# Performance work log

Measured on AMD Instinct MI355X. Metric: run time of the kernel, lower is better.

## Reference

```python
import jax, jax.numpy as jnp
import numpy as np

MAX_S, MIN_S, MAX_R = 3.0, 0.5, 3.0
A = (MAX_S - MIN_S) / 2.0   # 1.25
B = (MAX_S + MIN_S) / 2.0   # 1.75
C = (MAX_R - 1.0) / 2.0     # 1.0
D = (MAX_R + 1.0) / 2.0     # 2.0

# 3x3 kernel base points, row-major: dim0 = dy, dim1 = dx, shape [2, 9]
BASE = jnp.array([[-1, -1], [-1, 0], [-1, 1], [0, -1], [0, 0], [0, 1],
                  [1, -1], [1, 0], [1, 1]], dtype=jnp.float32).T


def conv2d(x, w, b=None):
    y = jax.lax.conv_general_dilated(x, w, window_strides=(1, 1),
                                     padding=((1, 1), (1, 1)),
                                     dimension_numbers=('NCHW', 'OIHW', 'NCHW'))
    if b is not None:
        y = y + b[None, :, None, None]
    return y


def setup_inputs() -> dict:
    key = jax.random.key(0)
    ks = jax.random.split(key, 8)
    return {
        'x': jax.random.normal(ks[0], (8, 64, 128, 128), jnp.float32),
        'w_main': jax.random.normal(ks[1], (64, 64, 3, 3), jnp.float32) * 0.05,
        'w_rot': jax.random.normal(ks[2], (2, 64, 3, 3), jnp.float32) * 0.05,
        'b_rot': jax.random.normal(ks[3], (2,), jnp.float32) * 0.05,
        'w_str': jax.random.normal(ks[4], (1, 64, 3, 3), jnp.float32) * 0.05,
        'b_str': jax.random.normal(ks[5], (1,), jnp.float32) * 0.05,
        'w_whl': jax.random.normal(ks[6], (1, 64, 3, 3), jnp.float32) * 0.05,
        'b_whl': jax.random.normal(ks[7], (1,), jnp.float32) * 0.05,
    }


def reference(x, w_main, w_rot, b_rot, w_str, b_str, w_whl, b_whl):
    b, c, H, W = x.shape
    K = 9
    # --- offset generation ---
    rot = conv2d(x, w_rot, b_rot)                     # [b,2,H,W]
    sin, cos = rot[:, 0], rot[:, 1]
    norm = jnp.sqrt(sin ** 2 + cos ** 2 + 1e-6)
    sin, cos = sin / norm, cos / norm
    r = jnp.tanh(conv2d(x, w_str, b_str))[:, 0] * A + B   # [b,H,W]
    wr = jnp.tanh(conv2d(x, w_whl, b_whl))[:, 0] * C + D  # [b,H,W]
    ky, kx = BASE[0], BASE[1]                             # [9]
    kyb = ky[None, :, None, None]
    kxb = kx[None, :, None, None]
    o0 = kyb * (wr * r)[:, None]                          # [b,9,H,W]
    o1 = kxb * wr[:, None]
    sinb, cosb = sin[:, None], cos[:, None]
    dy = cosb * o0 + sinb * o1 - kyb                      # rotation then subtract base
    dx = -sinb * o0 + cosb * o1 - kxb
    # --- deformable sampling positions (stride=1, pad=1, dil=1) ---
    py = jnp.arange(H, dtype=x.dtype)[None, None, :, None] + kyb + dy  # [b,9,H,W]
    px = jnp.arange(W, dtype=x.dtype)[None, None, None, :] + kxb + dx
    y0f = jnp.floor(py); x0f = jnp.floor(px)
    ly = py - y0f; lx = px - x0f
    y0 = y0f.astype(jnp.int32); x0 = x0f.astype(jnp.int32)
    x_flat = x.reshape(b, c, H * W)

    def gather(yi, xi, wgt):
        valid = (yi >= 0) & (yi < H) & (xi >= 0) & (xi < W)
        idx = jnp.clip(yi, 0, H - 1) * W + jnp.clip(xi, 0, W - 1)
        g = jnp.take_along_axis(x_flat, idx.reshape(b, 1, -1), axis=2)
        g = g.reshape(b, c, K, H, W)
        return g * (wgt * valid)[:, None]

    val = (gather(y0, x0, (1 - ly) * (1 - lx))
           + gather(y0, x0 + 1, (1 - ly) * lx)
           + gather(y0 + 1, x0, ly * (1 - lx))
           + gather(y0 + 1, x0 + 1, ly * lx))          # [b,c,9,H,W]
    # final 3x3 conv over sampled points == contraction over (c, k)
    out = jnp.einsum('bckhw,ock->bohw', val, w_main.reshape(w_main.shape[0], c, K))
    return out
```

## Files before the change

kernel.cpp:

```cpp
#include <hip/hip_runtime.h>
#include <hip/hip_bf16.h>
#include <math.h>

#define HH 128
#define WW 128
#define HWSZ (HH*WW)
#define CH 64
#define OC 64
#define NB 8
#define RG 28
#define RPX (RG*RG)

#define XT_BYTES   (16777216u)
#define OFFS_BYTES (2097152u)

typedef __attribute__((ext_vector_type(8))) short bf16x8_t;
typedef __attribute__((ext_vector_type(4))) float f32x4_t;

__global__ __launch_bounds__(256) void transpose_kernel(
    const float* __restrict__ x, const float* __restrict__ w_main,
    __hip_bfloat16* __restrict__ xT, __hip_bfloat16* __restrict__ wmT2)
{
    const int t = threadIdx.x;
    const int i = blockIdx.x;
    if (i >= 2048) {
        const int base = (i - 2048) * 4096 + t * 16;
        #pragma unroll
        for (int j = 0; j < 16; ++j) {
            const int e = base + j;
            const int k = e >> 12;
            const int r = e & 4095;
            const int o = r >> 6;
            const int c = r & 63;
            wmT2[e] = __float2bfloat16(w_main[(size_t)o * (CH * 9) + c * 9 + k]);
        }
        return;
    }
    __shared__ float tile[64][65];
    const int b = i & 7;
    const int j = i >> 3;
    const int h  = j >> 1;
    const int w0 = (j & 1) * 64;
    const float* xb = x + (size_t)b * CH * HWSZ + h * WW + w0;
    {
        const int w = t & 63, c0 = (t >> 6) * 16;
        #pragma unroll
        for (int jj = 0; jj < 16; ++jj)
            tile[c0 + jj][w] = xb[(size_t)(c0 + jj) * HWSZ + w];
    }
    __syncthreads();
    {
        const int c = t & 63, wq = t >> 6;
        __hip_bfloat16* o = xT + ((size_t)b * HWSZ + h * WW + w0) * 64;
        #pragma unroll
        for (int jj = 0; jj < 16; ++jj) {
            const int w = wq * 16 + jj;
            o[(size_t)w * 64 + c] = __float2bfloat16(tile[c][w]);
        }
    }
}

__global__ __launch_bounds__(256) void offsets_kernel(
    const float* __restrict__ x,
    const float* __restrict__ w_rot,
    const float* __restrict__ w_str,
    const float* __restrict__ w_whl,
    float* __restrict__ offs)
{
    __shared__ float xs[8][4][WW];
    const int t  = threadIdx.x;
    const int i  = blockIdx.x;
    const int b  = i & 7;
    const int rp = (i >> 3) & 63;
    const int cg = i >> 9;
    const int h0 = rp * 2;
    const int c0 = cg * 8;
    const float* xb = x + (size_t)b * CH * HWSZ;
    #pragma unroll
    for (int jj = 0; jj < 4; ++jj) {
        const int u   = t + jj * 256;
        const int ch  = u >> 7;
        const int rem = u & 127;
        const int row = rem >> 5;
        const int w4  = (rem & 31) * 4;
        const int grow = h0 - 1 + row;
        float4 v = make_float4(0.f, 0.f, 0.f, 0.f);
        if (grow >= 0 && grow < HH)
            v = *(const float4*)&xb[((size_t)(c0 + ch) * HH + grow) * WW + w4];
        *(float4*)&xs[ch][row][w4] = v;
    }
    __syncthreads();
    const int r = t >> 7, w = t & 127;
    const int wl = max(w - 1, 0), wr2 = min(w + 1, WW - 1);
    const float ml = (w > 0) ? 1.f : 0.f, mr = (w < WW - 1) ? 1.f : 0.f;
    float a0 = 0.f, a1 = 0.f, a2 = 0.f, a3 = 0.f;
    #pragma unroll
    for (int ch = 0; ch < 8; ++ch) {
        const int cc = c0 + ch;
        #pragma unroll
        for (int dy = 0; dy < 3; ++dy) {
            const float* row_ = &xs[ch][r + dy][0];
            const float nl = row_[wl] * ml;
            const float nc = row_[w];
            const float nr = row_[wr2] * mr;
            const int d0 = cc * 9 + dy * 3;
            a0 = fmaf(nl, w_rot[d0 + 0], a0); a0 = fmaf(nc, w_rot[d0 + 1], a0); a0 = fmaf(nr, w_rot[d0 + 2], a0);
            a1 = fmaf(nl, w_rot[576 + d0 + 0], a1); a1 = fmaf(nc, w_rot[576 + d0 + 1], a1); a1 = fmaf(nr, w_rot[576 + d0 + 2], a1);
            a2 = fmaf(nl, w_str[d0 + 0], a2); a2 = fmaf(nc, w_str[d0 + 1], a2); a2 = fmaf(nr, w_str[d0 + 2], a2);
            a3 = fmaf(nl, w_whl[d0 + 0], a3); a3 = fmaf(nc, w_whl[d0 + 1], a3); a3 = fmaf(nr, w_whl[d0 + 2], a3);
        }
    }
    float* op = &offs[(size_t)(b * HWSZ + (h0 + r) * WW + w) * 4];
    atomicAdd(op + 0, a0);
    atomicAdd(op + 1, a1);
    atomicAdd(op + 2, a2);
    atomicAdd(op + 3, a3);
}

__device__ __forceinline__ void bf2x(unsigned int u, float& lo, float& hi) {
    union { unsigned int v; float f; } a, b;
    a.v = u << 16; b.v = u & 0xFFFF0000u;
    lo = a.f; hi = b.f;
}

__device__ __forceinline__ void blend_mfma(
    const uint4& q00, const uint4& q01, const uint4& q10, const uint4& q11,
    float w00, float w01, float w10, float w11,
    const bf16x8_t& bf0, const bf16x8_t& bf1, const bf16x8_t& bf2v, const bf16x8_t& bf3,
    f32x4_t& acc0, f32x4_t& acc1, f32x4_t& acc2, f32x4_t& acc3)
{
    const unsigned int* u00 = (const unsigned int*)&q00;
    const unsigned int* u01 = (const unsigned int*)&q01;
    const unsigned int* u10 = (const unsigned int*)&q10;
    const unsigned int* u11 = (const unsigned int*)&q11;
    union { unsigned int u[4]; bf16x8_t v; } af;
    #pragma unroll
    for (int j = 0; j < 4; ++j) {
        float alo, ahi, blo, bhi, clo, chi, dlo, dhi;
        bf2x(u00[j], alo, ahi);
        bf2x(u01[j], blo, bhi);
        bf2x(u10[j], clo, chi);
        bf2x(u11[j], dlo, dhi);
        const float v_lo = w00 * alo + w01 * blo + w10 * clo + w11 * dlo;
        const float v_hi = w00 * ahi + w01 * bhi + w10 * chi + w11 * dhi;
        union { __hip_bfloat162 h; unsigned int u; } pk;
        pk.h = __float22bfloat162_rn(make_float2(v_lo, v_hi));
        af.u[j] = pk.u;
    }
    acc0 = __builtin_amdgcn_mfma_f32_16x16x32_bf16(af.v, bf0,  acc0, 0, 0, 0);
    acc1 = __builtin_amdgcn_mfma_f32_16x16x32_bf16(af.v, bf1,  acc1, 0, 0, 0);
    acc2 = __builtin_amdgcn_mfma_f32_16x16x32_bf16(af.v, bf2v, acc2, 0, 0, 0);
    acc3 = __builtin_amdgcn_mfma_f32_16x16x32_bf16(af.v, bf3,  acc3, 0, 0, 0);
}

__global__ __launch_bounds__(256, 3) void deform_kernel(
    const __hip_bfloat16* __restrict__ xT, const __hip_bfloat16* __restrict__ wmT2,
    const float* __restrict__ offs,
    const float* __restrict__ b_rot, const float* __restrict__ b_str,
    const float* __restrict__ b_whl, float* __restrict__ out)
{
    __shared__ union {
        uint4 xs[RPX * 4];
        float ots[64][67];
    } sh;
    const int t  = threadIdx.x;
    const int wv = t >> 6;
    const int l  = t & 63;
    const int lm = l & 15;
    const int lg = l >> 4;
    const int i  = blockIdx.x;
    const int b  = i & 7;
    const int tile = i >> 3;
    const int w0 = (tile & 15) * 8;
    const int h0 = (tile >> 4) * 8;
    const int pi = wv * 16 + lm;
    const int h = h0 + (pi >> 3);
    const int w = w0 + (pi & 7);
    const float4 o4 = *(const float4*)&offs[(size_t)(b * HWSZ + h * WW + w) * 4];
    float sv = o4.x + b_rot[0], cv = o4.y + b_rot[1];
    const float inv = 1.0f / sqrtf(sv * sv + cv * cv + 1e-6f);
    sv *= inv; cv *= inv;
    const float rr  = tanhf(o4.z + b_str[0]) * 1.25f + 1.75f;
    const float wq  = tanhf(o4.w + b_whl[0]) * 1.0f + 2.0f;
    const float av  = wq * rr;
    const float wvl = wq;
    const float hh  = (float)h;
    const float wwf = (float)w;
    const __hip_bfloat16* xb = xT + (size_t)b * HWSZ * 64;

    f32x4_t acc0 = {0.f, 0.f, 0.f, 0.f};
    f32x4_t acc1 = acc0, acc2 = acc0, acc3 = acc0;

    for (int g = 0; g < 2; ++g) {
        __syncthreads();
        for (int u = t; u < RPX * 4; u += 256) {
            const int pxu = u >> 2, q = u & 3;
            const int lr = pxu / RG;
            const int lc = pxu - lr * RG;
            const int gy = min(max(h0 - 10 + lr, 0), HH - 1);
            const int gx = min(max(w0 - 10 + lc, 0), WW - 1);
            sh.xs[pxu * 4 + q] =
                *(const uint4*)(xb + (size_t)(gy * WW + gx) * 64 + g * 32 + q * 8);
        }
        __syncthreads();
        const int cb0 = g * 32 + lg * 8;
        #pragma unroll
        for (int k = 0; k < 9; ++k) {
            const float kyf = (float)(k / 3) - 1.f;
            const float kxf = (float)(k % 3) - 1.f;
            const float o0v = kyf * av;
            const float o1v = kxf * wvl;
            const float pyf = hh  + cv * o0v + sv * o1v;
            const float pxf = wwf - sv * o0v + cv * o1v;
            const float y0f = floorf(pyf), x0f = floorf(pxf);
            const float ly = pyf - y0f, lx = pxf - x0f;
            const int y0 = (int)y0f, x0i = (int)x0f;
            const int y1 = y0 + 1, x1 = x0i + 1;
            const bool vy0 = (y0 >= 0) && (y0 < HH);
            const bool vy1 = (y1 >= 0) && (y1 < HH);
            const bool vx0 = (x0i >= 0) && (x0i < WW);
            const bool vx1 = (x1 >= 0) && (x1 < WW);
            const float w00 = (1.f - ly) * (1.f - lx) * ((vy0 && vx0) ? 1.f : 0.f);
            const float w01 = (1.f - ly) * lx         * ((vy0 && vx1) ? 1.f : 0.f);
            const float w10 = ly * (1.f - lx)         * ((vy1 && vx0) ? 1.f : 0.f);
            const float w11 = ly * lx                 * ((vy1 && vx1) ? 1.f : 0.f);
            const int ly0 = min(max(y0, 0), HH - 1) - (h0 - 10);
            const int ly1 = min(max(y1, 0), HH - 1) - (h0 - 10);
            const int lx0 = min(max(x0i, 0), WW - 1) - (w0 - 10);
            const int lx1 = min(max(x1, 0), WW - 1) - (w0 - 10);
            const uint4 q00 = sh.xs[(ly0 * RG + lx0) * 4 + lg];
            const uint4 q01 = sh.xs[(ly0 * RG + lx1) * 4 + lg];
            const uint4 q10 = sh.xs[(ly1 * RG + lx0) * 4 + lg];
            const uint4 q11 = sh.xs[(ly1 * RG + lx1) * 4 + lg];
            const __hip_bfloat16* wp = wmT2 + ((size_t)k * 64 + lm) * 64 + cb0;
            const bf16x8_t bf0 = *(const bf16x8_t*)(wp);
            const bf16x8_t bf1 = *(const bf16x8_t*)(wp + 1024);
            const bf16x8_t bf2v = *(const bf16x8_t*)(wp + 2048);
            const bf16x8_t bf3 = *(const bf16x8_t*)(wp + 3072);
            blend_mfma(q00, q01, q10, q11, w00, w01, w10, w11,
                       bf0, bf1, bf2v, bf3, acc0, acc1, acc2, acc3);
        }
    }
    __syncthreads();
    const int pxw = wv * 16 + lg * 4;
    #pragma unroll
    for (int rg2 = 0; rg2 < 4; ++rg2) {
        sh.ots[pxw + rg2][ 0 + lm] = acc0[rg2];
        sh.ots[pxw + rg2][16 + lm] = acc1[rg2];
        sh.ots[pxw + rg2][32 + lm] = acc2[rg2];
        sh.ots[pxw + rg2][48 + lm] = acc3[rg2];
    }
    __syncthreads();
    const int oo = t >> 2;
    const int q  = (t & 3) * 16;
    #pragma unroll
    for (int j2 = 0; j2 < 4; ++j2) {
        const int px = q + j2 * 4;
        float4 v = make_float4(sh.ots[px + 0][oo], sh.ots[px + 1][oo],
                               sh.ots[px + 2][oo], sh.ots[px + 3][oo]);
        *(float4*)&out[((size_t)b * OC + oo) * HWSZ +
                       (h0 + (px >> 3)) * WW + w0 + (px & 7)] = v;
    }
}

extern "C" void kernel_launch(void* const* d_in, const int* in_sizes, int n_in,
                              void* d_out, int out_size, void* d_ws, size_t ws_size,
                              hipStream_t stream)
{
    const float* x      = (const float*)d_in[0];
    const float* w_main = (const float*)d_in[1];
    const float* w_rot  = (const float*)d_in[2];
    const float* b_rot  = (const float*)d_in[3];
    const float* w_str  = (const float*)d_in[4];
    const float* b_str  = (const float*)d_in[5];
    const float* w_whl  = (const float*)d_in[6];
    const float* b_whl  = (const float*)d_in[7];
    float* out = (float*)d_out;

    char* ws = (char*)d_ws;
    __hip_bfloat16* xT   = (__hip_bfloat16*)ws;
    float*          offs = (float*)(ws + XT_BYTES);
    __hip_bfloat16* wmT2 = (__hip_bfloat16*)(ws + XT_BYTES + OFFS_BYTES);

    hipMemsetAsync(offs, 0, OFFS_BYTES, stream);
    transpose_kernel<<<dim3(2057), 256, 0, stream>>>(x, w_main, xT, wmT2);
    offsets_kernel<<<dim3(4096), 256, 0, stream>>>(x, w_rot, w_str, w_whl, offs);
    deform_kernel<<<dim3(2048), 256, 0, stream>>>(xT, wmT2, offs,
                                                  b_rot, b_str, b_whl, out);
}
```

Measured before the change: 252.3 us.

## Switch to fp16 packed blending, replace atomics with partial-sum reduce, swizzle LDS

Converts the staged activations and weights from bf16 to fp16 so the bilinear blend runs as packed half2 FMAs instead of unpacking to fp32 and repacking, and uses the fp16 MFMA. The offset conv writes per-channel-group partial sums into the output buffer as scratch, and a new reduce kernel sums them and applies bias, normalisation and tanh. This replaces the memset and the atomics. Bilinear weights and indices for all nine taps are precomputed once outside the channel-group loop, and the LDS tile uses an XOR swizzle to cut bank conflicts. In exchange, fp16 blending and storage lose accuracy, and holding the per-tap arrays adds register pressure.

New measurement: 211.1 us. 16.4% less time.

```diff
diff --git a/kernel.cpp b/kernel.cpp
--- a/kernel.cpp
+++ b/kernel.cpp
@@ -1,5 +1,6 @@
 #include <hip/hip_runtime.h>
 #include <hip/hip_bf16.h>
+#include <hip/hip_fp16.h>
 #include <math.h>
 
 #define HH 128
@@ -14,12 +15,12 @@
 #define XT_BYTES   (16777216u)
 #define OFFS_BYTES (2097152u)
 
-typedef __attribute__((ext_vector_type(8))) short bf16x8_t;
+typedef _Float16 f16x8 __attribute__((ext_vector_type(8)));
 typedef __attribute__((ext_vector_type(4))) float f32x4_t;
 
 __global__ __launch_bounds__(256) void transpose_kernel(
     const float* __restrict__ x, const float* __restrict__ w_main,
-    __hip_bfloat16* __restrict__ xT, __hip_bfloat16* __restrict__ wmT2)
+    __half* __restrict__ xT, __half* __restrict__ wmT2)
 {
     const int t = threadIdx.x;
     const int i = blockIdx.x;
@@ -32,7 +33,7 @@
             const int r = e & 4095;
             const int o = r >> 6;
             const int c = r & 63;
-            wmT2[e] = __float2bfloat16(w_main[(size_t)o * (CH * 9) + c * 9 + k]);
+            wmT2[e] = __float2half(w_main[(size_t)o * (CH * 9) + c * 9 + k]);
         }
         return;
     }
@@ -51,11 +52,11 @@
     __syncthreads();
     {
         const int c = t & 63, wq = t >> 6;
-        __hip_bfloat16* o = xT + ((size_t)b * HWSZ + h * WW + w0) * 64;
+        __half* o = xT + ((size_t)b * HWSZ + h * WW + w0) * 64;
         #pragma unroll
         for (int jj = 0; jj < 16; ++jj) {
             const int w = wq * 16 + jj;
-            o[(size_t)w * 64 + c] = __float2bfloat16(tile[c][w]);
+            o[(size_t)w * 64 + c] = __float2half(tile[c][w]);
         }
     }
 }
@@ -65,7 +66,7 @@
     const float* __restrict__ w_rot,
     const float* __restrict__ w_str,
     const float* __restrict__ w_whl,
-    float* __restrict__ offs)
+    float4* __restrict__ part)
 {
     __shared__ float xs[8][4][WW];
     const int t  = threadIdx.x;
@@ -110,54 +111,31 @@
             a3 = fmaf(nl, w_whl[d0 + 0], a3); a3 = fmaf(nc, w_whl[d0 + 1], a3); a3 = fmaf(nr, w_whl[d0 + 2], a3);
         }
     }
-    float* op = &offs[(size_t)(b * HWSZ + (h0 + r) * WW + w) * 4];
-    atomicAdd(op + 0, a0);
-    atomicAdd(op + 1, a1);
-    atomicAdd(op + 2, a2);
-    atomicAdd(op + 3, a3);
-}
-
-__device__ __forceinline__ void bf2x(unsigned int u, float& lo, float& hi) {
-    union { unsigned int v; float f; } a, b;
-    a.v = u << 16; b.v = u & 0xFFFF0000u;
-    lo = a.f; hi = b.f;
-}
-
-__device__ __forceinline__ void blend_mfma(
-    const uint4& q00, const uint4& q01, const uint4& q10, const uint4& q11,
-    float w00, float w01, float w10, float w11,
-    const bf16x8_t& bf0, const bf16x8_t& bf1, const bf16x8_t& bf2v, const bf16x8_t& bf3,
-    f32x4_t& acc0, f32x4_t& acc1, f32x4_t& acc2, f32x4_t& acc3)
-{
-    const unsigned int* u00 = (const unsigned int*)&q00;
-    const unsigned int* u01 = (const unsigned int*)&q01;
-    const unsigned int* u10 = (const unsigned int*)&q10;
-    const unsigned int* u11 = (const unsigned int*)&q11;
-    union { unsigned int u[4]; bf16x8_t v; } af;
-    #pragma unroll
-    for (int j = 0; j < 4; ++j) {
-        float alo, ahi, blo, bhi, clo, chi, dlo, dhi;
-        bf2x(u00[j], alo, ahi);
-        bf2x(u01[j], blo, bhi);
-        bf2x(u10[j], clo, chi);
-        bf2x(u11[j], dlo, dhi);
-        const float v_lo = w00 * alo + w01 * blo + w10 * clo + w11 * dlo;
-        const float v_hi = w00 * ahi + w01 * bhi + w10 * chi + w11 * dhi;
-        union { __hip_bfloat162 h; unsigned int u; } pk;
-        pk.h = __float22bfloat162_rn(make_float2(v_lo, v_hi));
-        af.u[j] = pk.u;
-    }
-    acc0 = __builtin_amdgcn_mfma_f32_16x16x32_bf16(af.v, bf0,  acc0, 0, 0, 0);
-    acc1 = __builtin_amdgcn_mfma_f32_16x16x32_bf16(af.v, bf1,  acc1, 0, 0, 0);
-    acc2 = __builtin_amdgcn_mfma_f32_16x16x32_bf16(af.v, bf2v, acc2, 0, 0, 0);
-    acc3 = __builtin_amdgcn_mfma_f32_16x16x32_bf16(af.v, bf3,  acc3, 0, 0, 0);
+    part[((size_t)cg * NB + b) * HWSZ + (h0 + r) * WW + w] = make_float4(a0, a1, a2, a3);
+}
+
+__global__ __launch_bounds__(256) void reduce_kernel(
+    const float4* __restrict__ part,
+    const float* __restrict__ b_rot, const float* __restrict__ b_str,
+    const float* __restrict__ b_whl, float4* __restrict__ offs)
+{
+    const int i = blockIdx.x * 256 + threadIdx.x;
+    float4 s = make_float4(0.f, 0.f, 0.f, 0.f);
+    #pragma unroll
+    for (int cg = 0; cg < 8; ++cg) {
+        const float4 p = part[(size_t)cg * NB * HWSZ + i];
+        s.x += p.x; s.y += p.y; s.z += p.z; s.w += p.w;
+    }
+    float sv = s.x + b_rot[0], cv = s.y + b_rot[1];
+    const float inv = 1.0f / sqrtf(sv * sv + cv * cv + 1e-6f);
+    const float rr = tanhf(s.z + b_str[0]) * 1.25f + 1.75f;
+    const float wq = tanhf(s.w + b_whl[0]) * 1.0f + 2.0f;
+    offs[i] = make_float4(sv * inv, cv * inv, wq * rr, wq);
 }
 
 __global__ __launch_bounds__(256, 3) void deform_kernel(
-    const __hip_bfloat16* __restrict__ xT, const __hip_bfloat16* __restrict__ wmT2,
-    const float* __restrict__ offs,
-    const float* __restrict__ b_rot, const float* __restrict__ b_str,
-    const float* __restrict__ b_whl, float* __restrict__ out)
+    const __half* __restrict__ xT, const __half* __restrict__ wmT2,
+    const float4* __restrict__ offs, float* __restrict__ out)
 {
     __shared__ union {
         uint4 xs[RPX * 4];
@@ -176,17 +154,39 @@
     const int pi = wv * 16 + lm;
     const int h = h0 + (pi >> 3);
     const int w = w0 + (pi & 7);
-    const float4 o4 = *(const float4*)&offs[(size_t)(b * HWSZ + h * WW + w) * 4];
-    float sv = o4.x + b_rot[0], cv = o4.y + b_rot[1];
-    const float inv = 1.0f / sqrtf(sv * sv + cv * cv + 1e-6f);
-    sv *= inv; cv *= inv;
-    const float rr  = tanhf(o4.z + b_str[0]) * 1.25f + 1.75f;
-    const float wq  = tanhf(o4.w + b_whl[0]) * 1.0f + 2.0f;
-    const float av  = wq * rr;
-    const float wvl = wq;
+    const float4 o4 = offs[(size_t)b * HWSZ + h * WW + w];
+    const float sv = o4.x, cv = o4.y, av = o4.z, wvl = o4.w;
     const float hh  = (float)h;
     const float wwf = (float)w;
-    const __hip_bfloat16* xb = xT + (size_t)b * HWSZ * 64;
+    const __half* xb = xT + (size_t)b * HWSZ * 64;
+
+    int ti[9], td[9];
+    __half2 w2[9][4];
+    #pragma unroll
+    for (int k = 0; k < 9; ++k) {
+        const float kyf = (float)(k / 3) - 1.f;
+        const float kxf = (float)(k % 3) - 1.f;
+        const float o0v = kyf * av;
+        const float o1v = kxf * wvl;
+        const float pyf = hh  + cv * o0v + sv * o1v;
+        const float pxf = wwf - sv * o0v + cv * o1v;
+        const float y0f = floorf(pyf), x0f = floorf(pxf);
+        const float ly = pyf - y0f, lx = pxf - x0f;
+        const int y0 = (int)y0f, x0i = (int)x0f;
+        const int y1 = y0 + 1, x1 = x0i + 1;
+        const bool vy0 = (y0 >= 0) && (y0 < HH);
+        const bool vy1 = (y1 >= 0) && (y1 < HH);
+        const bool vx0 = (x0i >= 0) && (x0i < WW);
+        const bool vx1 = (x1 >= 0) && (x1 < WW);
+        w2[k][0] = __float2half2_rn((1.f - ly) * (1.f - lx) * ((vy0 && vx0) ? 1.f : 0.f));
+        w2[k][1] = __float2half2_rn((1.f - ly) * lx         * ((vy0 && vx1) ? 1.f : 0.f));
+        w2[k][2] = __float2half2_rn(ly * (1.f - lx)         * ((vy1 && vx0) ? 1.f : 0.f));
+        w2[k][3] = __float2half2_rn(ly * lx                 * ((vy1 && vx1) ? 1.f : 0.f));
+        const int iy0 = min(max(y0, 0), HH - 1), iy1 = min(max(y1, 0), HH - 1);
+        const int ix0 = min(max(x0i, 0), WW - 1), ix1 = min(max(x1, 0), WW - 1);
+        ti[k] = (iy0 - (h0 - 10)) * RG + (ix0 - (w0 - 10));
+        td[k] = (ix1 - ix0) | ((iy1 - iy0) << 1);
+    }
 
     f32x4_t acc0 = {0.f, 0.f, 0.f, 0.f};
     f32x4_t acc1 = acc0, acc2 = acc0, acc3 = acc0;
@@ -199,46 +199,42 @@
             const int lc = pxu - lr * RG;
             const int gy = min(max(h0 - 10 + lr, 0), HH - 1);
             const int gx = min(max(w0 - 10 + lc, 0), WW - 1);
-            sh.xs[pxu * 4 + q] =
+            sh.xs[pxu * 4 + (q ^ (pxu & 3))] =
                 *(const uint4*)(xb + (size_t)(gy * WW + gx) * 64 + g * 32 + q * 8);
         }
         __syncthreads();
         const int cb0 = g * 32 + lg * 8;
         #pragma unroll
         for (int k = 0; k < 9; ++k) {
-            const float kyf = (float)(k / 3) - 1.f;
-            const float kxf = (float)(k % 3) - 1.f;
-            const float o0v = kyf * av;
-            const float o1v = kxf * wvl;
-            const float pyf = hh  + cv * o0v + sv * o1v;
-            const float pxf = wwf - sv * o0v + cv * o1v;
-            const float y0f = floorf(pyf), x0f = floorf(pxf);
-            const float ly = pyf - y0f, lx = pxf - x0f;
-            const int y0 = (int)y0f, x0i = (int)x0f;
-            const int y1 = y0 + 1, x1 = x0i + 1;
-            const bool vy0 = (y0 >= 0) && (y0 < HH);
-            const bool vy1 = (y1 >= 0) && (y1 < HH);
-            const bool vx0 = (x0i >= 0) && (x0i < WW);
-            const bool vx1 = (x1 >= 0) && (x1 < WW);
-            const float w00 = (1.f - ly) * (1.f - lx) * ((vy0 && vx0) ? 1.f : 0.f);
-            const float w01 = (1.f - ly) * lx         * ((vy0 && vx1) ? 1.f : 0.f);
-            const float w10 = ly * (1.f - lx)         * ((vy1 && vx0) ? 1.f : 0.f);
-            const float w11 = ly * lx                 * ((vy1 && vx1) ? 1.f : 0.f);
-            const int ly0 = min(max(y0, 0), HH - 1) - (h0 - 10);
-            const int ly1 = min(max(y1, 0), HH - 1) - (h0 - 10);
-            const int lx0 = min(max(x0i, 0), WW - 1) - (w0 - 10);
-            const int lx1 = min(max(x1, 0), WW - 1) - (w0 - 10);
-            const uint4 q00 = sh.xs[(ly0 * RG + lx0) * 4 + lg];
-            const uint4 q01 = sh.xs[(ly0 * RG + lx1) * 4 + lg];
-            const uint4 q10 = sh.xs[(ly1 * RG + lx0) * 4 + lg];
-            const uint4 q11 = sh.xs[(ly1 * RG + lx1) * 4 + lg];
-            const __hip_bfloat16* wp = wmT2 + ((size_t)k * 64 + lm) * 64 + cb0;
-            const bf16x8_t bf0 = *(const bf16x8_t*)(wp);
-            const bf16x8_t bf1 = *(const bf16x8_t*)(wp + 1024);
-            const bf16x8_t bf2v = *(const bf16x8_t*)(wp + 2048);
-            const bf16x8_t bf3 = *(const bf16x8_t*)(wp + 3072);
-            blend_mfma(q00, q01, q10, q11, w00, w01, w10, w11,
-                       bf0, bf1, bf2v, bf3, acc0, acc1, acc2, acc3);
+            const int i00 = ti[k];
+            const int dxx = td[k] & 1;
+            const int dyy = (td[k] >> 1) * RG;
+            const int i01 = i00 + dxx;
+            const int i10 = i00 + dyy;
+            const int i11 = i10 + dxx;
+            union Q { uint4 q; __half2 h2[4]; };
+            Q q00, q01, q10, q11;
+            q00.q = sh.xs[i00 * 4 + (lg ^ (i00 & 3))];
+            q01.q = sh.xs[i01 * 4 + (lg ^ (i01 & 3))];
+            q10.q = sh.xs[i10 * 4 + (lg ^ (i10 & 3))];
+            q11.q = sh.xs[i11 * 4 + (lg ^ (i11 & 3))];
+            union { __half2 h2[4]; f16x8 v; } af;
+            #pragma unroll
+            for (int j = 0; j < 4; ++j) {
+                af.h2[j] = __hfma2(q00.h2[j], w2[k][0],
+                           __hfma2(q01.h2[j], w2[k][1],
+                           __hfma2(q10.h2[j], w2[k][2],
+                           __hmul2(q11.h2[j], w2[k][3]))));
+            }
+            const __half* wp = wmT2 + ((size_t)k * 64 + lm) * 64 + cb0;
+            const f16x8 bf0 = *(const f16x8*)(wp);
+            const f16x8 bf1 = *(const f16x8*)(wp + 1024);
+            const f16x8 bf2v = *(const f16x8*)(wp + 2048);
+            const f16x8 bf3 = *(const f16x8*)(wp + 3072);
+            acc0 = __builtin_amdgcn_mfma_f32_16x16x32_f16(af.v, bf0,  acc0, 0, 0, 0);
+            acc1 = __builtin_amdgcn_mfma_f32_16x16x32_f16(af.v, bf1,  acc1, 0, 0, 0);
+            acc2 = __builtin_amdgcn_mfma_f32_16x16x32_f16(af.v, bf2v, acc2, 0, 0, 0);
+            acc3 = __builtin_amdgcn_mfma_f32_16x16x32_f16(af.v, bf3,  acc3, 0, 0, 0);
         }
     }
     __syncthreads();
@@ -278,13 +274,14 @@
     float* out = (float*)d_out;
 
     char* ws = (char*)d_ws;
-    __hip_bfloat16* xT   = (__hip_bfloat16*)ws;
-    float*          offs = (float*)(ws + XT_BYTES);
-    __hip_bfloat16* wmT2 = (__hip_bfloat16*)(ws + XT_BYTES + OFFS_BYTES);
-
-    hipMemsetAsync(offs, 0, OFFS_BYTES, stream);
+    __half*  xT   = (__half*)ws;
+    float4*  offs = (float4*)(ws + XT_BYTES);
+    __half*  wmT2 = (__half*)(ws + XT_BYTES + OFFS_BYTES);
+    float4*  part = (float4*)d_out;
+
     transpose_kernel<<<dim3(2057), 256, 0, stream>>>(x, w_main, xT, wmT2);
-    offsets_kernel<<<dim3(4096), 256, 0, stream>>>(x, w_rot, w_str, w_whl, offs);
-    deform_kernel<<<dim3(2048), 256, 0, stream>>>(xT, wmT2, offs,
-                                                  b_rot, b_str, b_whl, out);
-}
+    offsets_kernel<<<dim3(4096), 256, 0, stream>>>(x, w_rot, w_str, w_whl, part);
+    reduce_kernel<<<dim3(NB * HWSZ / 256), 256, 0, stream>>>(
+        part, b_rot, b_str, b_whl, offs);
+    deform_kernel<<<dim3(2048), 256, 0, stream>>>(xT, wmT2, offs, out);
+}
```
